# Optimization experiments

Measured on AMD Instinct MI355X. Metric: run time of the kernel, lower is better.

The kernel has to match this reference:

```python
import jax, jax.numpy as jnp
import numpy as np

K = 3  # kernel_size

def setup_inputs() -> dict:
    key = jax.random.key(0)
    k1, k2, k3 = jax.random.split(key, 3)
    B, C, H, W = 8, 64, 128, 128
    x = jax.random.normal(k1, (B, C, H, W), dtype=jnp.float32)
    # 1x1 conv weight (out_channels*K*K, in_channels) and bias
    W_gen = jax.random.normal(k2, (C * K * K, C), dtype=jnp.float32) / np.float32(np.sqrt(C))
    b_gen = jax.random.normal(k3, (C * K * K,), dtype=jnp.float32) * 0.01
    return {"x": x, "W_gen": W_gen, "b_gen": b_gen}

def reference(x, W_gen, b_gen):
    B, C, H, W = x.shape  # out_channels == in_channels (required by the view)
    # filter_gen: 1x1 conv + ReLU -> (B, C*K*K, H, W)
    f = jax.nn.relu(jnp.einsum('bchw,oc->bohw', x, W_gen) + b_gen[None, :, None, None])
    filters = f.reshape(B, C, K * K, H, W)
    # F.unfold with padding=(K-1)//2, stride 1: gather KxK patches per pixel.
    pad = (K - 1) // 2
    xp = jnp.pad(x, ((0, 0), (0, 0), (pad, pad), (pad, pad)))
    # kernel-position index runs row-major (i*K + j), matching unfold layout
    patches = jnp.stack([xp[:, :, i:i + H, j:j + W]
                         for i in range(K) for j in range(K)], axis=2)  # (B,C,K*K,H,W)
    out = (filters * patches).sum(axis=2)  # (B,C,H,W)
    return out
```

## Files before the change

kernel.cpp:

```cpp
#include <hip/hip_runtime.h>
#include <hip/hip_bf16.h>

#define CC 64
#define HH 128
#define WW 128
#define OO 576
#define HW (HH * WW)

typedef __attribute__((ext_vector_type(8))) short short8;
typedef __attribute__((ext_vector_type(4))) float floatx4;

__device__ __forceinline__ unsigned short f2bf(float f) {
    unsigned u = __float_as_uint(f);
    u = (u + 0x7FFFu + ((u >> 16) & 1u)) >> 16;
    return (unsigned short)u;
}

__global__ void ACDA_wconv_kernel(const float* __restrict__ Wg,
                                  unsigned short* __restrict__ Wb) {
    int i = blockIdx.x * 256 + threadIdx.x;
    if (i < OO * CC) {
        int o2  = i >> 6;
        int col = i & 63;
        int kk  = o2 >> 6;
        int c   = o2 & 63;
        Wb[i] = f2bf(Wg[(c * 9 + kk) * CC + col]);
    }
}

__global__ __launch_bounds__(256, 4) void ACDA_main_kernel(
    const float* __restrict__ x, const unsigned short* __restrict__ Wb,
    const float* __restrict__ bg, float* __restrict__ out)
{
    __shared__ __align__(16) char smem[20480];
    float (*FbufT)[64][20] = reinterpret_cast<float(*)[64][20]>(smem);
    unsigned short (*Bl)[72] = reinterpret_cast<unsigned short(*)[72]>(smem);

    const int tid  = threadIdx.x;
    const int lane = tid & 63;
    const int wv   = tid >> 6;
    const int quad = lane >> 4;
    const int l16  = lane & 15;
    const int c0   = wv * 16;

    const int bid = blockIdx.x;
    const int wk  = (bid & 7) * 256 + (bid >> 3);
    const int seg = wk & 1;
    const int h   = (wk >> 1) & 127;
    const int b   = wk >> 8;
    const int w0  = seg << 6;

    const float* xb = x + (size_t)b * CC * HW;

    int wA = w0 + lane - 1; bool badA = (wA < 0);   if (badA) wA = 0;
    int wB = w0 + lane;
    int wC = w0 + lane + 1; bool badC = (wC > 127); if (badC) wC = 127;
    const int soffC = c0 * HW;

    {
        const int w = w0 + lane;
#pragma unroll
        for (int cc = 0; cc < 16; cc += 2) {
            const int c = c0 + cc;
            float f0 = xb[(c * HH + h) * WW + w];
            float f1 = xb[((c + 1) * HH + h) * WW + w];
            __hip_bfloat162 p = __float22bfloat162_rn(make_float2(f0, f1));
            unsigned u;
            __builtin_memcpy(&u, &p, 4);
            *(unsigned*)&Bl[lane][c] = u;
        }
    }

    float oacc[16];
#pragma unroll
    for (int i = 0; i < 16; ++i) oacc[i] = 0.f;

    short8 a0A, a1A, a0B, a1B;
    floatx4 bvA, bvB;
#define LOADA(KK, A0, A1, BV) do {                                          \
        const unsigned short* wrow_ = Wb + ((KK) * 64 + c0 + l16) * CC + quad * 8; \
        (A0) = *(const short8*)(wrow_);                                     \
        (A1) = *(const short8*)(wrow_ + 32);                                \
        const float* bp_ = bg + (c0 + quad * 4) * 9 + (KK);                 \
        (BV)[0] = bp_[0]; (BV)[1] = bp_[9];                                 \
        (BV)[2] = bp_[18]; (BV)[3] = bp_[27];                               \
    } while (0)

    LOADA(0, a0A, a1A, bvA);

    __syncthreads();

    short8 bfrag[4][2];
#pragma unroll
    for (int nt = 0; nt < 4; ++nt)
#pragma unroll
        for (int ks = 0; ks < 2; ++ks)
            bfrag[nt][ks] = *(const short8*)&Bl[nt * 16 + l16][ks * 32 + quad * 8];

    __syncthreads();

#define BODY(KK, A0C, A1C, BVC, A0N, A1N, BVN, PREF) do {                   \
        if (PREF) LOADA((KK) + 1, A0N, A1N, BVN);                           \
        const int di_ = (KK) < 3 ? 0 : ((KK) < 6 ? 1 : 2);                  \
        const int dj_ = (KK) - 3 * di_;                                     \
        int rr_ = h + di_ - 1;                                              \
        const bool rbad_ = (rr_ < 0) || (rr_ > 127);                        \
        rr_ = rr_ < 0 ? 0 : (rr_ > 127 ? 127 : rr_);                        \
        const int  wsel_ = (dj_ == 0) ? wA : ((dj_ == 1) ? wB : wC);        \
        const bool wbad_ = (dj_ == 0) ? badA : ((dj_ == 2) ? badC : false); \
        const bool badk_ = rbad_ || wbad_;                                  \
        const int  pbk_  = soffC + rr_ * WW + wsel_;                        \
        float pv_[16];                                                      \
        _Pragma("unroll")                                                   \
        for (int r_ = 0; r_ < 16; ++r_) pv_[r_] = xb[pbk_ + r_ * HW];       \
        _Pragma("unroll")                                                   \
        for (int nt_ = 0; nt_ < 4; ++nt_) {                                 \
            floatx4 z_ = (BVC);      \
            z_ = __builtin_amdgcn_mfma_f32_16x16x32_bf16((A0C), bfrag[nt_][0], z_, 0, 0, 0); \
            z_ = __builtin_amdgcn_mfma_f32_16x16x32_bf16((A1C), bfrag[nt_][1], z_, 0, 0, 0); \
            *(floatx4*)&FbufT[wv][nt_ * 16 + l16][quad * 4] = z_;           \
        }                                                                   \
        _Pragma("unroll")                                                   \
        for (int g_ = 0; g_ < 4; ++g_) {                                    \
            floatx4 f4_ = *(const floatx4*)&FbufT[wv][lane][g_ * 4];        \
            _Pragma("unroll")                                               \
            for (int rr2_ = 0; rr2_ < 4; ++rr2_) {                          \
                const int r_ = g_ * 4 + rr2_;                               \
                float fv_ = fmaxf(f4_[rr2_], 0.f);                          \
                float pvv_ = badk_ ? 0.f : pv_[r_];                         \
                oacc[r_] = fmaf(fv_, pvv_, oacc[r_]);                       \
            }                                                               \
        }                                                                   \
    } while (0)

#pragma unroll 1
    for (int kk = 0; kk < 8; kk += 2) {
        BODY(kk,     a0A, a1A, bvA, a0B, a1B, bvB, true);
        BODY(kk + 1, a0B, a1B, bvB, a0A, a1A, bvA, true);
    }
    BODY(8, a0A, a1A, bvA, a0B, a1B, bvB, false);

#undef BODY
#undef LOADA

    float* ob = out + (size_t)b * CC * HW + h * WW + w0 + lane;
#pragma unroll
    for (int i = 0; i < 16; ++i)
        ob[(c0 + i) * HW] = oacc[i];
}

extern "C" void kernel_launch(void* const* d_in, const int* in_sizes, int n_in,
                              void* d_out, int out_size, void* d_ws, size_t ws_size,
                              hipStream_t stream) {
    const float* x  = (const float*)d_in[0];
    const float* Wg = (const float*)d_in[1];
    const float* bg = (const float*)d_in[2];
    float* out = (float*)d_out;
    unsigned short* Wb = (unsigned short*)d_ws;

    ACDA_wconv_kernel<<<dim3((OO * CC + 255) / 256), dim3(256), 0, stream>>>(Wg, Wb);
    ACDA_main_kernel<<<dim3(8 * 128 * 2), dim3(256), 0, stream>>>(x, Wb, bg, out);
}
```

Measured before the change: 113.6 us.

## Stage 3-row input halo tile in LDS and consume MFMA output in registers

Each block now loads the three input rows (all 64 channels plus left and right halo columns) into a padded fp32 LDS tile once. The MFMA B fragments and all nine shifted patch values are read from that tile instead of issuing 16 global loads per kernel position. The epilogue keeps the MFMA accumulator layout in registers and drops the FbufT round-trip through shared memory, with output stores remapped to match. The tile needs about 52KB of LDS per block, which may cut the number of resident blocks below the launch-bounds target.

```diff
diff --git a/kernel.cpp b/kernel.cpp
--- a/kernel.cpp
+++ b/kernel.cpp
@@ -32,9 +32,8 @@
     const float* __restrict__ x, const unsigned short* __restrict__ Wb,
     const float* __restrict__ bg, float* __restrict__ out)
 {
-    __shared__ __align__(16) char smem[20480];
-    float (*FbufT)[64][20] = reinterpret_cast<float(*)[64][20]>(smem);
-    unsigned short (*Bl)[72] = reinterpret_cast<unsigned short(*)[72]>(smem);
+    __shared__ float S[3][64][68];
+    float* Sf = &S[0][0][0];
 
     const int tid  = threadIdx.x;
     const int lane = tid & 63;
@@ -52,28 +51,56 @@
 
     const float* xb = x + (size_t)b * CC * HW;
 
-    int wA = w0 + lane - 1; bool badA = (wA < 0);   if (badA) wA = 0;
-    int wB = w0 + lane;
-    int wC = w0 + lane + 1; bool badC = (wC > 127); if (badC) wC = 127;
-    const int soffC = c0 * HW;
-
     {
-        const int w = w0 + lane;
-#pragma unroll
-        for (int cc = 0; cc < 16; cc += 2) {
-            const int c = c0 + cc;
-            float f0 = xb[(c * HH + h) * WW + w];
-            float f1 = xb[((c + 1) * HH + h) * WW + w];
-            __hip_bfloat162 p = __float22bfloat162_rn(make_float2(f0, f1));
-            unsigned u;
-            __builtin_memcpy(&u, &p, 4);
-            *(unsigned*)&Bl[lane][c] = u;
+        const int colT = tid & 63;
+        const int row0 = tid >> 6;
+#pragma unroll 8
+        for (int it = 0; it < 48; ++it) {
+            const int row = it * 4 + row0;
+            const int di  = row >> 6;
+            const int c   = row & 63;
+            int hh = h + di - 1; hh = hh < 0 ? 0 : (hh > 127 ? 127 : hh);
+            Sf[row * 68 + colT + 1] = xb[c * HW + hh * WW + w0 + colT];
+        }
+        if (tid < 192) {
+            const int di = tid >> 6;
+            const int c  = tid & 63;
+            int hh = h + di - 1; hh = hh < 0 ? 0 : (hh > 127 ? 127 : hh);
+            const int base = c * HW + hh * WW;
+            int colL = w0 - 1;  if (colL < 0)   colL = 0;
+            int colR = w0 + 64; if (colR > 127) colR = 127;
+            Sf[tid * 68]      = xb[base + colL];
+            Sf[tid * 68 + 65] = xb[base + colR];
         }
     }
+    __syncthreads();
 
-    float oacc[16];
+    short8 bfrag[4][2];
 #pragma unroll
-    for (int i = 0; i < 16; ++i) oacc[i] = 0.f;
+    for (int nt = 0; nt < 4; ++nt)
+#pragma unroll
+        for (int ks = 0; ks < 2; ++ks) {
+            short8 v;
+#pragma unroll
+            for (int j = 0; j < 8; j += 2) {
+                const int c = ks * 32 + quad * 8 + j;
+                float f0 = Sf[(64 + c) * 68 + nt * 16 + l16 + 1];
+                float f1 = Sf[(64 + c + 1) * 68 + nt * 16 + l16 + 1];
+                __hip_bfloat162 p = __float22bfloat162_rn(make_float2(f0, f1));
+                unsigned u;
+                __builtin_memcpy(&u, &p, 4);
+                v[j]     = (short)(u & 0xffffu);
+                v[j + 1] = (short)(u >> 16);
+            }
+            bfrag[nt][ks] = v;
+        }
+
+    floatx4 acc[4];
+#pragma unroll
+    for (int nt = 0; nt < 4; ++nt) acc[nt] = floatx4{0.f, 0.f, 0.f, 0.f};
+
+    const bool fc = (w0 + l16 == 0);
+    const bool lc = (w0 + l16 == 79);
 
     short8 a0A, a1A, a0B, a1B;
     floatx4 bvA, bvB;
@@ -88,47 +115,37 @@
 
     LOADA(0, a0A, a1A, bvA);
 
-    __syncthreads();
-
-    short8 bfrag[4][2];
-#pragma unroll
-    for (int nt = 0; nt < 4; ++nt)
-#pragma unroll
-        for (int ks = 0; ks < 2; ++ks)
-            bfrag[nt][ks] = *(const short8*)&Bl[nt * 16 + l16][ks * 32 + quad * 8];
-
-    __syncthreads();
-
 #define BODY(KK, A0C, A1C, BVC, A0N, A1N, BVN, PREF) do {                   \
         if (PREF) LOADA((KK) + 1, A0N, A1N, BVN);                           \
         const int di_ = (KK) < 3 ? 0 : ((KK) < 6 ? 1 : 2);                  \
         const int dj_ = (KK) - 3 * di_;                                     \
-        int rr_ = h + di_ - 1;                                              \
-        const bool rbad_ = (rr_ < 0) || (rr_ > 127);                        \
-        rr_ = rr_ < 0 ? 0 : (rr_ > 127 ? 127 : rr_);                        \
-        const int  wsel_ = (dj_ == 0) ? wA : ((dj_ == 1) ? wB : wC);        \
-        const bool wbad_ = (dj_ == 0) ? badA : ((dj_ == 2) ? badC : false); \
-        const bool badk_ = rbad_ || wbad_;                                  \
-        const int  pbk_  = soffC + rr_ * WW + wsel_;                        \
-        float pv_[16];                                                      \
+        const int hh_ = h + di_ - 1;                                        \
+        const bool rbad_ = (hh_ < 0) || (hh_ > 127);                        \
+        const int base_ = (di_ * 64 + c0 + 4 * quad) * 68 + l16 + dj_;      \
+        float pv_[4][4];                                                    \
         _Pragma("unroll")                                                   \
-        for (int r_ = 0; r_ < 16; ++r_) pv_[r_] = xb[pbk_ + r_ * HW];       \
+        for (int nt_ = 0; nt_ < 4; ++nt_)                                   \
+            _Pragma("unroll")                                               \
+            for (int rg_ = 0; rg_ < 4; ++rg_)                               \
+                pv_[nt_][rg_] = Sf[base_ + rg_ * 68 + nt_ * 16];            \
+        floatx4 z_[4];                                                      \
         _Pragma("unroll")                                                   \
         for (int nt_ = 0; nt_ < 4; ++nt_) {                                 \
-            floatx4 z_ = (BVC);      \
-            z_ = __builtin_amdgcn_mfma_f32_16x16x32_bf16((A0C), bfrag[nt_][0], z_, 0, 0, 0); \
-            z_ = __builtin_amdgcn_mfma_f32_16x16x32_bf16((A1C), bfrag[nt_][1], z_, 0, 0, 0); \
-            *(floatx4*)&FbufT[wv][nt_ * 16 + l16][quad * 4] = z_;           \
+            floatx4 t_ = (BVC);      \
+            t_ = __builtin_amdgcn_mfma_f32_16x16x32_bf16((A0C), bfrag[nt_][0], t_, 0, 0, 0); \
+            t_ = __builtin_amdgcn_mfma_f32_16x16x32_bf16((A1C), bfrag[nt_][1], t_, 0, 0, 0); \
+            z_[nt_] = t_;                                                   \
         }                                                                   \
+        const bool kA_ = (dj_ == 0) && fc;                                  \
+        const bool kC_ = (dj_ == 2) && lc;                                  \
         _Pragma("unroll")                                                   \
-        for (int g_ = 0; g_ < 4; ++g_) {                                    \
-            floatx4 f4_ = *(const floatx4*)&FbufT[wv][lane][g_ * 4];        \
+        for (int nt_ = 0; nt_ < 4; ++nt_) {                                 \
             _Pragma("unroll")                                               \
-            for (int rr2_ = 0; rr2_ < 4; ++rr2_) {                          \
-                const int r_ = g_ * 4 + rr2_;                               \
-                float fv_ = fmaxf(f4_[rr2_], 0.f);                          \
-                float pvv_ = badk_ ? 0.f : pv_[r_];                         \
-                oacc[r_] = fmaf(fv_, pvv_, oacc[r_]);                       \
+            for (int rg_ = 0; rg_ < 4; ++rg_) {                             \
+                float fv_ = fmaxf(z_[nt_][rg_], 0.f);                       \
+                const bool kill_ = rbad_ || (nt_ == 0 && kA_) || (nt_ == 3 && kC_); \
+                float pvv_ = kill_ ? 0.f : pv_[nt_][rg_];                   \
+                acc[nt_][rg_] = fmaf(fv_, pvv_, acc[nt_][rg_]);             \
             }                                                               \
         }                                                                   \
     } while (0)
@@ -143,10 +160,12 @@
 #undef BODY
 #undef LOADA
 
-    float* ob = out + (size_t)b * CC * HW + h * WW + w0 + lane;
+    float* ob = out + (size_t)b * CC * HW + h * WW + w0;
 #pragma unroll
-    for (int i = 0; i < 16; ++i)
-        ob[(c0 + i) * HW] = oacc[i];
+    for (int nt = 0; nt < 4; ++nt)
+#pragma unroll
+        for (int rg = 0; rg < 4; ++rg)
+            ob[(c0 + 4 * quad + rg) * HW + nt * 16 + l16] = acc[nt][rg];
 }
 
 extern "C" void kernel_launch(void* const* d_in, const int* in_sizes, int n_in,
```

New measurement: 113.4 us. Within noise of the previous version (-0.1%).
